# Performance work log

Hardware: AMD Instinct MI355X
Metric: run time of the kernel (lower is better)

Reference implementation:

```python
import jax, jax.numpy as jnp
import numpy as np

H = 256   # hidden_dim
S = 16    # d_state
B = 2
N = 8192
LN_EPS = 1e-5


def setup_inputs() -> dict:
    key = jax.random.key(0)
    ks = jax.random.split(key, 12)
    std = 1.0 / np.sqrt(H)
    inp = {
        'x': jax.random.normal(ks[0], (B, N, H), dtype=jnp.float32),
        'in_w': jax.random.normal(ks[1], (2 * H, H), dtype=jnp.float32) * std,
        'in_b': jax.random.normal(ks[2], (2 * H,), dtype=jnp.float32) * std,
        'xp_w': jax.random.normal(ks[3], (2 * S + 1, H), dtype=jnp.float32) * std,
        'xp_b': jax.random.normal(ks[4], (2 * S + 1,), dtype=jnp.float32) * std,
        'dt_w': jax.random.normal(ks[5], (H, 1), dtype=jnp.float32),
        'dt_b': jax.random.normal(ks[6], (H,), dtype=jnp.float32),
        'A_log': jnp.log(jnp.broadcast_to(jnp.arange(1, S + 1, dtype=jnp.float32), (H, S))),
        'D': jnp.ones((H,), dtype=jnp.float32),
        'out_w': jax.random.normal(ks[7], (H, H), dtype=jnp.float32) * std,
        'out_b': jax.random.normal(ks[8], (H,), dtype=jnp.float32) * std,
        'ln_g': jnp.ones((H,), dtype=jnp.float32),
        'ln_b': jnp.zeros((H,), dtype=jnp.float32),
    }
    return inp


def reference(x, in_w, in_b, xp_w, xp_b, dt_w, dt_b, A_log, D, out_w, out_b, ln_g, ln_b):
    # x: (B, N, H). Dropout is identity in eval mode.
    residual = x
    xz = jnp.einsum('bnh,kh->bnk', x, in_w) + in_b            # (B,N,2H)
    x_inner, z = xz[..., :H], xz[..., H:]
    x_dbl = jnp.einsum('bnh,kh->bnk', x_inner, xp_w) + xp_b   # (B,N,2S+1)
    dt_raw = x_dbl[..., :1]
    B_raw = x_dbl[..., 1:S + 1]                               # (B,N,S)
    C_raw = x_dbl[..., S + 1:]                                # (B,N,S)
    dt = jax.nn.softplus(dt_raw * dt_w[:, 0] + dt_b)          # (B,N,H)
    # NOTE: the original computes dA = exp(dt * A) but never uses it; A_log
    # does not affect the output, so we skip materializing dA.
    dB = dt[..., None] * B_raw[:, :, None, :]                 # (B,N,H,S)
    h = jnp.cumsum(x_inner[..., None] * dB, axis=1)           # (B,N,H,S)
    y = jnp.einsum('bnhs,bns->bnh', h, C_raw) + D * x_inner   # (B,N,H)
    y = y * jax.nn.silu(z)
    out = jnp.einsum('bnh,kh->bnk', y, out_w) + out_b
    r = out + residual
    mu = jnp.mean(r, axis=-1, keepdims=True)
    var = jnp.mean((r - mu) ** 2, axis=-1, keepdims=True)
    return ln_g * (r - mu) * jax.lax.rsqrt(var + LN_EPS) + ln_b
```

## Files before the change

### kernel.cpp

```cpp
#include <hip/hip_runtime.h>
#include <hip/hip_bf16.h>


#define HD 256
#define SD 16
#define NSEQ 8192
#define NBATCH 2
#define BN (NBATCH * NSEQ)
#define CHUNK 32
#define NCHUNK (NSEQ / CHUNK)
#define NGRP 16
#define GSZ (NCHUNK / NGRP)
#define LN_EPS 1e-5f
#define UST 40
#define PST 257

#define NIW (2 * HD * HD)
#define NXP (48 * HD)
#define NOW (HD * HD)

typedef __hip_bfloat16 bf16;
typedef __attribute__((ext_vector_type(8))) short bf16x8;
typedef __attribute__((ext_vector_type(4))) short short4v;
typedef __attribute__((ext_vector_type(4))) float f32x4;
typedef __attribute__((ext_vector_type(4))) unsigned int uint4v;
typedef __attribute__((ext_vector_type(2))) unsigned int uint2v;

__device__ __forceinline__ float b2f(bf16 v) { return __bfloat162float(v); }
__device__ __forceinline__ short f2bs(float f) {
  union { bf16 b; short s; } u;
  u.b = __float2bfloat16(f);
  return u.s;
}
__device__ __forceinline__ unsigned int pack2(float a, float b) {
  return (unsigned int)(unsigned short)f2bs(a) |
         ((unsigned int)(unsigned short)f2bs(b) << 16);
}
__device__ __forceinline__ bf16x8 cvt_frag(const float* p) {
  bf16x8 r;
#pragma unroll
  for (int j = 0; j < 8; ++j) r[j] = f2bs(p[j]);
  return r;
}
__device__ __forceinline__ float softplus_f(float a) {
  return (a > 20.f) ? a : __logf(1.f + __expf(a));
}

__global__ __launch_bounds__(256) void k0_weights(
    const float* __restrict__ in_w, const float* __restrict__ xp_w,
    const float* __restrict__ out_w, bf16* __restrict__ wbin,
    bf16* __restrict__ wbxp, bf16* __restrict__ wbout)
{
  const int base = (blockIdx.x * 256 + threadIdx.x) * 4;
  if (base < NIW) {
    f32x4 v = *(const f32x4*)(in_w + base);
    *(short4v*)((short*)wbin + base) =
        short4v{f2bs(v[0]), f2bs(v[1]), f2bs(v[2]), f2bs(v[3])};
  } else if (base < NIW + NXP) {
    const int off = base - NIW;
    short4v s;
    if (off < 33 * HD) {
      f32x4 v = *(const f32x4*)(xp_w + off);
      s = short4v{f2bs(v[0]), f2bs(v[1]), f2bs(v[2]), f2bs(v[3])};
    } else {
      s = short4v{0, 0, 0, 0};
    }
    *(short4v*)((short*)wbxp + off) = s;
  } else if (base < NIW + NXP + NOW) {
    const int off = base - NIW - NXP;
    f32x4 v = *(const f32x4*)(out_w + off);
    *(short4v*)((short*)wbout + off) =
        short4v{f2bs(v[0]), f2bs(v[1]), f2bs(v[2]), f2bs(v[3])};
  }
}

__global__ __launch_bounds__(256) void k1_gemm(
    const float* __restrict__ x, const bf16* __restrict__ wbin,
    const float* __restrict__ in_b, bf16* __restrict__ xib,
    bf16* __restrict__ zb)
{
  __shared__ __align__(16) char smem[128 * 264 * 2];
  bf16* At = (bf16*)smem;
  float* Ct = (float*)smem;

  const int tid = threadIdx.x;
  const int rt = blockIdx.x & 127, ct = blockIdx.x >> 7;
  const int R0 = rt * 128, C0 = ct * 128;
  const int wave = tid >> 6, lane = tid & 63, q = lane >> 4, l16 = lane & 15;

#pragma unroll
  for (int it = 0; it < 16; ++it) {
    const int f = tid + it * 256;
    const int row = f >> 5, g = f & 31;
    bf16x8 v = cvt_frag(x + (size_t)(R0 + row) * HD + g * 8);
    *(bf16x8*)(At + row * 264 + g * 8) = v;
  }
  __syncthreads();

  const int rowHalf = (wave & 1) * 64;
  const int colHalf = (wave >> 1) * 64;
  f32x4 acc[4][4] = {};
  const bf16* bp = wbin + (size_t)(C0 + colHalf + l16) * HD + q * 8;
#pragma unroll
  for (int k = 0; k < HD; k += 32) {
    bf16x8 a[4], b[4];
#pragma unroll
    for (int i = 0; i < 4; ++i)
      a[i] = *(const bf16x8*)(At + (rowHalf + i * 16 + l16) * 264 + k + q * 8);
#pragma unroll
    for (int j = 0; j < 4; ++j)
      b[j] = *(const bf16x8*)(bp + (size_t)j * 16 * HD + k);
#pragma unroll
    for (int i = 0; i < 4; ++i)
#pragma unroll
      for (int j = 0; j < 4; ++j)
        acc[i][j] = __builtin_amdgcn_mfma_f32_16x16x32_bf16(a[i], b[j], acc[i][j], 0, 0, 0);
  }
  __syncthreads();

#pragma unroll
  for (int j = 0; j < 4; ++j) {
    const int col = colHalf + j * 16 + l16;
    const float bias = in_b[C0 + col];
#pragma unroll
    for (int i = 0; i < 4; ++i)
#pragma unroll
      for (int r = 0; r < 4; ++r)
        Ct[(rowHalf + i * 16 + q * 4 + r) * 132 + col] = acc[i][j][r] + bias;
  }
  __syncthreads();

  bf16* dst = (C0 < HD) ? xib : zb;
  const int Cd = (C0 < HD) ? C0 : (C0 - HD);
#pragma unroll
  for (int it = 0; it < 8; ++it) {
    const int f = tid + it * 256;
    const int row = f >> 4, g = f & 15;
    bf16x8 v = cvt_frag(Ct + row * 132 + g * 8);
    *(bf16x8*)(dst + (size_t)(R0 + row) * HD + Cd + g * 8) = v;
  }
}

__global__ __launch_bounds__(256) void kS_xp_sum(
    const bf16* __restrict__ xib, const bf16* __restrict__ wbxp,
    const float* __restrict__ xp_b, const float* __restrict__ dt_w,
    const float* __restrict__ dt_b, float* __restrict__ dbc,
    float* __restrict__ Mc)
{
  __shared__ __align__(16) bf16 xt[32 * 264];
  __shared__ __align__(16) bf16 wp[48 * 264];
  __shared__ __align__(16) float sdbc[32][33];
  __shared__ __align__(16) bf16 sBt[16 * UST];
  __shared__ __align__(16) bf16 Ut[256 * UST];
  const int tid = threadIdx.x;
  const int wave = tid >> 6, lane = tid & 63, q = lane >> 4, l16 = lane & 15;
  const int cix = blockIdx.x;
  const int R0 = cix * CHUNK;

#pragma unroll
  for (int it = 0; it < 4; ++it) {
    const int f = tid + it * 256, row = f >> 5, g = f & 31;
    *(bf16x8*)(xt + row * 264 + g * 8) =
        *(const bf16x8*)(xib + (size_t)(R0 + row) * HD + g * 8);
  }
#pragma unroll
  for (int it = 0; it < 6; ++it) {
    const int f = tid + it * 256, row = f >> 5, g = f & 31;
    *(bf16x8*)(wp + row * 264 + g * 8) =
        *(const bf16x8*)(wbxp + (size_t)row * HD + g * 8);
  }
  __syncthreads();

  if (wave < 2) {
    f32x4 pacc[3] = {};
#pragma unroll
    for (int k = 0; k < HD; k += 32) {
      bf16x8 af = *(const bf16x8*)(xt + (wave * 16 + l16) * 264 + k + q * 8);
#pragma unroll
      for (int t = 0; t < 3; ++t) {
        bf16x8 bfr = *(const bf16x8*)(wp + (t * 16 + l16) * 264 + k + q * 8);
        pacc[t] = __builtin_amdgcn_mfma_f32_16x16x32_bf16(af, bfr, pacc[t], 0, 0, 0);
      }
    }
#pragma unroll
    for (int t = 0; t < 3; ++t) {
      const int col = t * 16 + l16;
      if (col < 33) {
        const float bias = xp_b[col];
#pragma unroll
        for (int r = 0; r < 4; ++r) {
          const int row = wave * 16 + q * 4 + r;
          const float v = pacc[t][r] + bias;
          sdbc[row][col] = v;
          if (col >= 1 && col < 17)
            *((short*)sBt + (col - 1) * UST + row) = f2bs(v);
        }
      }
    }
  }
  __syncthreads();

  {
    const float* sflat = &sdbc[0][0];
    for (int idx = tid; idx < CHUNK * 33; idx += 256)
      dbc[(size_t)R0 * 33 + idx] = sflat[idx];
  }
  {
    const int h = tid;
    const float dtw = dt_w[h], dtb = dt_b[h];
    unsigned int up[16];
#pragma unroll
    for (int n2 = 0; n2 < 16; ++n2) {
      const int n = 2 * n2;
      const float xv0 = b2f(xt[n * 264 + h]);
      const float xv1 = b2f(xt[(n + 1) * 264 + h]);
      const float u0 = xv0 * softplus_f(sdbc[n][0] * dtw + dtb);
      const float u1 = xv1 * softplus_f(sdbc[n + 1][0] * dtw + dtb);
      up[n2] = pack2(u0, u1);
    }
    uint4v* dst = (uint4v*)(Ut + h * UST);
#pragma unroll
    for (int j = 0; j < 4; ++j)
      dst[j] = uint4v{up[4 * j], up[4 * j + 1], up[4 * j + 2], up[4 * j + 3]};
  }
  __syncthreads();

  {
    bf16x8 af = *(const bf16x8*)(sBt + l16 * UST + q * 8);
    f32x4 macc[4] = {};
#pragma unroll
    for (int c4 = 0; c4 < 4; ++c4) {
      const int ct = wave * 4 + c4;
      bf16x8 bu = *(const bf16x8*)(Ut + (ct * 16 + l16) * UST + q * 8);
      macc[c4] = __builtin_amdgcn_mfma_f32_16x16x32_bf16(af, bu, macc[c4], 0, 0, 0);
    }
    float* mbase = Mc + (size_t)cix * 4096;
#pragma unroll
    for (int c4 = 0; c4 < 4; ++c4) {
      const int h = (wave * 4 + c4) * 16 + l16;
#pragma unroll
      for (int r = 0; r < 4; ++r)
        mbase[(q * 4 + r) * HD + h] = macc[c4][r];
    }
  }
}

__global__ __launch_bounds__(256) void k4a_prefix_local(
    float* __restrict__ Mc, float* __restrict__ Gs)
{
  const int tid = blockIdx.x * 256 + threadIdx.x;
  const int b = tid >> 16;
  const int g = (tid >> 12) & (NGRP - 1);
  const int hs = tid & 4095;
  float run = 0.f;
#pragma unroll
  for (int i = 0; i < GSZ; ++i) {
    const size_t idx = ((size_t)(b * NCHUNK + g * GSZ + i)) * 4096 + hs;
    const float v = Mc[idx];
    Mc[idx] = run;
    run += v;
  }
  Gs[((size_t)(b * NGRP + g)) * 4096 + hs] = run;
}

__global__ __launch_bounds__(256) void k4b_prefix_groups(float* __restrict__ Gs)
{
  const int tid = blockIdx.x * 256 + threadIdx.x;
  const int b = tid >> 12;
  const int hs = tid & 4095;
  float run = 0.f;
#pragma unroll
  for (int g = 0; g < NGRP; ++g) {
    const size_t idx = ((size_t)(b * NGRP + g)) * 4096 + hs;
    const float v = Gs[idx];
    Gs[idx] = run;
    run += v;
  }
}

__global__ __launch_bounds__(256) void k56_scan_out_ln(
    const bf16* __restrict__ xib, const bf16* __restrict__ zb,
    const float* __restrict__ dbc, const float* __restrict__ dt_w,
    const float* __restrict__ dt_b, const float* __restrict__ Dv,
    const float* __restrict__ Mc, const float* __restrict__ Gs,
    const bf16* __restrict__ wbout, const float* __restrict__ out_b,
    const float* __restrict__ x, const float* __restrict__ ln_g,
    const float* __restrict__ ln_b, float* __restrict__ out)
{
  __shared__ __align__(16) char un[53376];
  bf16* Ut  = (bf16*)un;
  bf16* Hst = (bf16*)(un + 20480);
  bf16* Ctl = (bf16*)(un + 40960);
  bf16* Tt  = (bf16*)(un + 43520);
  bf16* yb  = (bf16*)un;
  float* pt = (float*)(un + 20480);
  __shared__ float sdbc[32][33];

  const int tid = threadIdx.x;
  const int wave = tid >> 6, lane = tid & 63, q = lane >> 4, l16 = lane & 15;
  const int cix = blockIdx.x;
  const int R0 = cix * CHUNK;
  const int b = cix >> 8;
  const int cchunk = cix & 255;

  {
    float* sflat = &sdbc[0][0];
    for (int idx = tid; idx < CHUNK * 33; idx += 256)
      sflat[idx] = dbc[(size_t)R0 * 33 + idx];
  }
  __syncthreads();

  {
    const int n = tid >> 3;
    const int m0 = (tid & 7) * 4;
    float cn[SD];
#pragma unroll
    for (int s = 0; s < SD; ++s) cn[s] = sdbc[n][17 + s];
    short4v tv;
#pragma unroll
    for (int mm = 0; mm < 4; ++mm) {
      const int m = m0 + mm;
      float t = 0.f;
#pragma unroll
      for (int s = 0; s < SD; ++s) t += cn[s] * sdbc[m][1 + s];
      tv[mm] = (m <= n) ? f2bs(t) : (short)0;
    }
    *(short4v*)((short*)Tt + n * 32 + m0) = tv;
  }
  {
    const int n = tid >> 3, k0 = (tid & 7) * 4;
    float v[4];
#pragma unroll
    for (int j = 0; j < 4; ++j) {
      const int k = k0 + j;
      v[j] = (k < SD) ? sdbc[n][17 + k] : 0.f;
    }
    *(uint2v*)((short*)Ctl + n * UST + k0) = uint2v{pack2(v[0], v[1]), pack2(v[2], v[3])};
  }
  {
    const int h = tid;
    const float* mp = Mc + (size_t)cix * 4096 + h;
    const float* gp = Gs + ((size_t)(b * NGRP + cchunk / GSZ)) * 4096 + h;
    unsigned int hp[8];
#pragma unroll
    for (int s2 = 0; s2 < 8; ++s2) {
      const int s = 2 * s2;
      hp[s2] = pack2(mp[s * HD] + gp[s * HD], mp[(s + 1) * HD] + gp[(s + 1) * HD]);
    }
    uint4v* hd = (uint4v*)(Hst + h * UST);
    hd[0] = uint4v{hp[0], hp[1], hp[2], hp[3]};
    hd[1] = uint4v{hp[4], hp[5], hp[6], hp[7]};
    hd[2] = uint4v{0, 0, 0, 0};
    hd[3] = uint4v{0, 0, 0, 0};
  }
  {
    const int h = tid;
    const float dtw = dt_w[h], dtb = dt_b[h];
    unsigned int up[16];
#pragma unroll
    for (int n2 = 0; n2 < 16; ++n2) {
      const int n = 2 * n2;
      const float xv0 = b2f(xib[(size_t)(R0 + n) * HD + h]);
      const float xv1 = b2f(xib[(size_t)(R0 + n + 1) * HD + h]);
      const float u0 = xv0 * softplus_f(sdbc[n][0] * dtw + dtb);
      const float u1 = xv1 * softplus_f(sdbc[n + 1][0] * dtw + dtb);
      up[n2] = pack2(u0, u1);
    }
    uint4v* dst = (uint4v*)(Ut + h * UST);
#pragma unroll
    for (int j = 0; j < 4; ++j)
      dst[j] = uint4v{up[4 * j], up[4 * j + 1], up[4 * j + 2], up[4 * j + 3]};
  }
  __syncthreads();

  f32x4 acc[2][4] = {};
  {
    bf16x8 aT0 = *(const bf16x8*)(Tt + l16 * 32 + q * 8);
    bf16x8 aT1 = *(const bf16x8*)(Tt + (16 + l16) * 32 + q * 8);
    bf16x8 aC0 = *(const bf16x8*)(Ctl + l16 * UST + q * 8);
    bf16x8 aC1 = *(const bf16x8*)(Ctl + (16 + l16) * UST + q * 8);
#pragma unroll
    for (int c4 = 0; c4 < 4; ++c4) {
      const int ct = wave * 4 + c4;
      bf16x8 bu = *(const bf16x8*)(Ut + (ct * 16 + l16) * UST + q * 8);
      bf16x8 bh = *(const bf16x8*)(Hst + (ct * 16 + l16) * UST + q * 8);
      acc[0][c4] = __builtin_amdgcn_mfma_f32_16x16x32_bf16(aT0, bu, acc[0][c4], 0, 0, 0);
      acc[0][c4] = __builtin_amdgcn_mfma_f32_16x16x32_bf16(aC0, bh, acc[0][c4], 0, 0, 0);
      acc[1][c4] = __builtin_amdgcn_mfma_f32_16x16x32_bf16(aT1, bu, acc[1][c4], 0, 0, 0);
      acc[1][c4] = __builtin_amdgcn_mfma_f32_16x16x32_bf16(aC1, bh, acc[1][c4], 0, 0, 0);
    }
  }
  __syncthreads();

  {
#pragma unroll
    for (int c4 = 0; c4 < 4; ++c4) {
      const int h = (wave * 4 + c4) * 16 + l16;
      const float dh = Dv[h];
#pragma unroll
      for (int rt = 0; rt < 2; ++rt)
#pragma unroll
        for (int r = 0; r < 4; ++r) {
          const int n = rt * 16 + q * 4 + r;
          const size_t grow = (size_t)(R0 + n) * HD + h;
          const float xv = b2f(xib[grow]);
          const float zv = b2f(zb[grow]);
          const float yv = acc[rt][c4][r] + dh * xv;
          const float sig = 1.f / (1.f + __expf(-zv));
          ((short*)yb)[n * 264 + h] = f2bs(yv * zv * sig);
        }
    }
  }
  __syncthreads();

  const int cw = wave * 64;
  f32x4 oacc[2][4] = {};
#pragma unroll
  for (int k = 0; k < HD; k += 32) {
    bf16x8 a0 = *(const bf16x8*)(yb + l16 * 264 + k + q * 8);
    bf16x8 a1 = *(const bf16x8*)(yb + (16 + l16) * 264 + k + q * 8);
#pragma unroll
    for (int t = 0; t < 4; ++t) {
      bf16x8 bfr = *(const bf16x8*)(wbout + (size_t)(cw + t * 16 + l16) * HD + k + q * 8);
      oacc[0][t] = __builtin_amdgcn_mfma_f32_16x16x32_bf16(a0, bfr, oacc[0][t], 0, 0, 0);
      oacc[1][t] = __builtin_amdgcn_mfma_f32_16x16x32_bf16(a1, bfr, oacc[1][t], 0, 0, 0);
    }
  }
#pragma unroll
  for (int t = 0; t < 4; ++t) {
    const int col = cw + t * 16 + l16;
    const float bias = out_b[col];
#pragma unroll
    for (int rt = 0; rt < 2; ++rt)
#pragma unroll
      for (int r = 0; r < 4; ++r) {
        const int row = rt * 16 + q * 4 + r;
        pt[row * PST + col] = oacc[rt][t][r] + bias + x[(size_t)(R0 + row) * HD + col];
      }
  }
  __syncthreads();

#pragma unroll
  for (int rr = 0; rr < 8; ++rr) {
    const int row = wave * 8 + rr;
    float p = 0.f;
#pragma unroll
    for (int j = 0; j < 4; ++j) p += pt[row * PST + lane + 64 * j];
#pragma unroll
    for (int off = 32; off > 0; off >>= 1) p += __shfl_xor(p, off);
    const float mu = p * (1.f / 256.f);
    float v2 = 0.f;
#pragma unroll
    for (int j = 0; j < 4; ++j) {
      const float d = pt[row * PST + lane + 64 * j] - mu;
      v2 += d * d;
    }
#pragma unroll
    for (int off = 32; off > 0; off >>= 1) v2 += __shfl_xor(v2, off);
    const float rstd = rsqrtf(v2 * (1.f / 256.f) + LN_EPS);
    const size_t base = (size_t)(R0 + row) * HD;
#pragma unroll
    for (int j = 0; j < 4; ++j) {
      const int cc = lane + 64 * j;
      out[base + cc] = ln_g[cc] * (pt[row * PST + cc] - mu) * rstd + ln_b[cc];
    }
  }
}

extern "C" void kernel_launch(void* const* d_in, const int* in_sizes, int n_in,
                              void* d_out, int out_size, void* d_ws, size_t ws_size,
                              hipStream_t stream)
{
  const float* x     = (const float*)d_in[0];
  const float* in_w  = (const float*)d_in[1];
  const float* in_b  = (const float*)d_in[2];
  const float* xp_w  = (const float*)d_in[3];
  const float* xp_b  = (const float*)d_in[4];
  const float* dt_w  = (const float*)d_in[5];
  const float* dt_b  = (const float*)d_in[6];
  const float* Dv    = (const float*)d_in[8];
  const float* out_w = (const float*)d_in[9];
  const float* out_b = (const float*)d_in[10];
  const float* ln_g  = (const float*)d_in[11];
  const float* ln_b  = (const float*)d_in[12];

  char* ws = (char*)d_ws;
  bf16*  xib   = (bf16*)(ws);
  bf16*  zb    = (bf16*)(ws +  8388608);
  float* dbc   = (float*)(ws + 16777216);
  float* Mc    = (float*)(ws + 18939904);
  float* Gs    = (float*)(ws + 27328512);
  bf16*  wbin  = (bf16*)(ws + 27852800);
  bf16*  wbxp  = (bf16*)(ws + 28114944);
  bf16*  wbout = (bf16*)(ws + 28139520);
  float* out   = (float*)d_out;

  hipLaunchKernelGGL(k0_weights, dim3((NIW + NXP + NOW) / 1024), dim3(256),
                     0, stream, in_w, xp_w, out_w, wbin, wbxp, wbout);
  hipLaunchKernelGGL(k1_gemm, dim3(512), dim3(256), 0, stream,
                     x, wbin, in_b, xib, zb);
  hipLaunchKernelGGL(kS_xp_sum, dim3(BN / CHUNK), dim3(256), 0, stream,
                     xib, wbxp, xp_b, dt_w, dt_b, dbc, Mc);
  hipLaunchKernelGGL(k4a_prefix_local, dim3(NBATCH * NGRP * 4096 / 256),
                     dim3(256), 0, stream, Mc, Gs);
  hipLaunchKernelGGL(k4b_prefix_groups, dim3(NBATCH * 4096 / 256), dim3(256),
                     0, stream, Gs);
  hipLaunchKernelGGL(k56_scan_out_ln, dim3(BN / CHUNK), dim3(256), 0, stream,
                     xib, zb, dbc, dt_w, dt_b, Dv, Mc, Gs,
                     wbout, out_b, x, ln_g, ln_b, out);
}
```

Measured before the change: 142.1 us.

## Double block size to 512 threads in GEMM, chunk-sum and scan-output kernels

Three main kernels move from 256 to 512 threads per block, and the work is repartitioned across eight waves instead of four. In the input GEMM each wave now owns a 32x64 tile, while the scan and output kernels split the state and time dimensions across two thread halves. The goal is more wavefronts per block to hide latency, plus smaller per-thread register tiles. The cost is that each wave gets less MFMA work to amortise its fragment loads, and the larger blocks may limit how many blocks fit on a CU.

```diff
diff --git a/kernel.cpp b/kernel.cpp
--- a/kernel.cpp
+++ b/kernel.cpp
@@ -24,7 +24,6 @@
 typedef __attribute__((ext_vector_type(4))) short short4v;
 typedef __attribute__((ext_vector_type(4))) float f32x4;
 typedef __attribute__((ext_vector_type(4))) unsigned int uint4v;
-typedef __attribute__((ext_vector_type(2))) unsigned int uint2v;
 
 __device__ __forceinline__ float b2f(bf16 v) { return __bfloat162float(v); }
 __device__ __forceinline__ short f2bs(float f) {
@@ -74,7 +73,7 @@
   }
 }
 
-__global__ __launch_bounds__(256) void k1_gemm(
+__global__ __launch_bounds__(512) void k1_gemm(
     const float* __restrict__ x, const bf16* __restrict__ wbin,
     const float* __restrict__ in_b, bf16* __restrict__ xib,
     bf16* __restrict__ zb)
@@ -89,29 +88,29 @@
   const int wave = tid >> 6, lane = tid & 63, q = lane >> 4, l16 = lane & 15;
 
 #pragma unroll
-  for (int it = 0; it < 16; ++it) {
-    const int f = tid + it * 256;
+  for (int it = 0; it < 8; ++it) {
+    const int f = tid + it * 512;
     const int row = f >> 5, g = f & 31;
     bf16x8 v = cvt_frag(x + (size_t)(R0 + row) * HD + g * 8);
     *(bf16x8*)(At + row * 264 + g * 8) = v;
   }
   __syncthreads();
 
-  const int rowHalf = (wave & 1) * 64;
-  const int colHalf = (wave >> 1) * 64;
-  f32x4 acc[4][4] = {};
-  const bf16* bp = wbin + (size_t)(C0 + colHalf + l16) * HD + q * 8;
+  const int rowQ = (wave & 3) * 32;
+  const int colH = (wave >> 2) * 64;
+  f32x4 acc[2][4] = {};
+  const bf16* bp = wbin + (size_t)(C0 + colH + l16) * HD + q * 8;
 #pragma unroll
   for (int k = 0; k < HD; k += 32) {
-    bf16x8 a[4], b[4];
-#pragma unroll
-    for (int i = 0; i < 4; ++i)
-      a[i] = *(const bf16x8*)(At + (rowHalf + i * 16 + l16) * 264 + k + q * 8);
+    bf16x8 a[2], b[4];
+#pragma unroll
+    for (int i = 0; i < 2; ++i)
+      a[i] = *(const bf16x8*)(At + (rowQ + i * 16 + l16) * 264 + k + q * 8);
 #pragma unroll
     for (int j = 0; j < 4; ++j)
       b[j] = *(const bf16x8*)(bp + (size_t)j * 16 * HD + k);
 #pragma unroll
-    for (int i = 0; i < 4; ++i)
+    for (int i = 0; i < 2; ++i)
 #pragma unroll
       for (int j = 0; j < 4; ++j)
         acc[i][j] = __builtin_amdgcn_mfma_f32_16x16x32_bf16(a[i], b[j], acc[i][j], 0, 0, 0);
@@ -120,28 +119,28 @@
 
 #pragma unroll
   for (int j = 0; j < 4; ++j) {
-    const int col = colHalf + j * 16 + l16;
+    const int col = colH + j * 16 + l16;
     const float bias = in_b[C0 + col];
 #pragma unroll
-    for (int i = 0; i < 4; ++i)
+    for (int i = 0; i < 2; ++i)
 #pragma unroll
       for (int r = 0; r < 4; ++r)
-        Ct[(rowHalf + i * 16 + q * 4 + r) * 132 + col] = acc[i][j][r] + bias;
+        Ct[(rowQ + i * 16 + q * 4 + r) * 132 + col] = acc[i][j][r] + bias;
   }
   __syncthreads();
 
   bf16* dst = (C0 < HD) ? xib : zb;
   const int Cd = (C0 < HD) ? C0 : (C0 - HD);
 #pragma unroll
-  for (int it = 0; it < 8; ++it) {
-    const int f = tid + it * 256;
+  for (int it = 0; it < 4; ++it) {
+    const int f = tid + it * 512;
     const int row = f >> 4, g = f & 15;
     bf16x8 v = cvt_frag(Ct + row * 132 + g * 8);
     *(bf16x8*)(dst + (size_t)(R0 + row) * HD + Cd + g * 8) = v;
   }
 }
 
-__global__ __launch_bounds__(256) void kS_xp_sum(
+__global__ __launch_bounds__(512) void kS_xp_sum(
     const bf16* __restrict__ xib, const bf16* __restrict__ wbxp,
     const float* __restrict__ xp_b, const float* __restrict__ dt_w,
     const float* __restrict__ dt_b, float* __restrict__ dbc,
@@ -158,14 +157,14 @@
   const int R0 = cix * CHUNK;
 
 #pragma unroll
-  for (int it = 0; it < 4; ++it) {
-    const int f = tid + it * 256, row = f >> 5, g = f & 31;
+  for (int it = 0; it < 2; ++it) {
+    const int f = tid + it * 512, row = f >> 5, g = f & 31;
     *(bf16x8*)(xt + row * 264 + g * 8) =
         *(const bf16x8*)(xib + (size_t)(R0 + row) * HD + g * 8);
   }
 #pragma unroll
-  for (int it = 0; it < 6; ++it) {
-    const int f = tid + it * 256, row = f >> 5, g = f & 31;
+  for (int it = 0; it < 3; ++it) {
+    const int f = tid + it * 512, row = f >> 5, g = f & 31;
     *(bf16x8*)(wp + row * 264 + g * 8) =
         *(const bf16x8*)(wbxp + (size_t)row * HD + g * 8);
   }
@@ -202,45 +201,45 @@
 
   {
     const float* sflat = &sdbc[0][0];
-    for (int idx = tid; idx < CHUNK * 33; idx += 256)
+    for (int idx = tid; idx < CHUNK * 33; idx += 512)
       dbc[(size_t)R0 * 33 + idx] = sflat[idx];
   }
   {
-    const int h = tid;
+    const int h = tid & 255;
+    const int sh = tid >> 8;
     const float dtw = dt_w[h], dtb = dt_b[h];
-    unsigned int up[16];
-#pragma unroll
-    for (int n2 = 0; n2 < 16; ++n2) {
-      const int n = 2 * n2;
+    unsigned int up[8];
+#pragma unroll
+    for (int n2 = 0; n2 < 8; ++n2) {
+      const int n = sh * 16 + 2 * n2;
       const float xv0 = b2f(xt[n * 264 + h]);
       const float xv1 = b2f(xt[(n + 1) * 264 + h]);
       const float u0 = xv0 * softplus_f(sdbc[n][0] * dtw + dtb);
       const float u1 = xv1 * softplus_f(sdbc[n + 1][0] * dtw + dtb);
       up[n2] = pack2(u0, u1);
     }
-    uint4v* dst = (uint4v*)(Ut + h * UST);
-#pragma unroll
-    for (int j = 0; j < 4; ++j)
-      dst[j] = uint4v{up[4 * j], up[4 * j + 1], up[4 * j + 2], up[4 * j + 3]};
+    uint4v* dst = (uint4v*)(Ut + h * UST + sh * 16);
+    dst[0] = uint4v{up[0], up[1], up[2], up[3]};
+    dst[1] = uint4v{up[4], up[5], up[6], up[7]};
   }
   __syncthreads();
 
   {
     bf16x8 af = *(const bf16x8*)(sBt + l16 * UST + q * 8);
-    f32x4 macc[4] = {};
-#pragma unroll
-    for (int c4 = 0; c4 < 4; ++c4) {
-      const int ct = wave * 4 + c4;
+    f32x4 macc[2] = {};
+#pragma unroll
+    for (int c2 = 0; c2 < 2; ++c2) {
+      const int ct = wave * 2 + c2;
       bf16x8 bu = *(const bf16x8*)(Ut + (ct * 16 + l16) * UST + q * 8);
-      macc[c4] = __builtin_amdgcn_mfma_f32_16x16x32_bf16(af, bu, macc[c4], 0, 0, 0);
+      macc[c2] = __builtin_amdgcn_mfma_f32_16x16x32_bf16(af, bu, macc[c2], 0, 0, 0);
     }
     float* mbase = Mc + (size_t)cix * 4096;
 #pragma unroll
-    for (int c4 = 0; c4 < 4; ++c4) {
-      const int h = (wave * 4 + c4) * 16 + l16;
+    for (int c2 = 0; c2 < 2; ++c2) {
+      const int h = (wave * 2 + c2) * 16 + l16;
 #pragma unroll
       for (int r = 0; r < 4; ++r)
-        mbase[(q * 4 + r) * HD + h] = macc[c4][r];
+        mbase[(q * 4 + r) * HD + h] = macc[c2][r];
     }
   }
 }
@@ -278,7 +277,7 @@
   }
 }
 
-__global__ __launch_bounds__(256) void k56_scan_out_ln(
+__global__ __launch_bounds__(512) void k56_scan_out_ln(
     const bf16* __restrict__ xib, const bf16* __restrict__ zb,
     const float* __restrict__ dbc, const float* __restrict__ dt_w,
     const float* __restrict__ dt_b, const float* __restrict__ Dv,
@@ -304,98 +303,91 @@
   const int cchunk = cix & 255;
 
   {
-    float* sflat = &sdbc[0][0];
-    for (int idx = tid; idx < CHUNK * 33; idx += 256)
-      sflat[idx] = dbc[(size_t)R0 * 33 + idx];
-  }
-  __syncthreads();
-
-  {
-    const int n = tid >> 3;
-    const int m0 = (tid & 7) * 4;
-    float cn[SD];
-#pragma unroll
-    for (int s = 0; s < SD; ++s) cn[s] = sdbc[n][17 + s];
-    short4v tv;
-#pragma unroll
-    for (int mm = 0; mm < 4; ++mm) {
-      const int m = m0 + mm;
-      float t = 0.f;
-#pragma unroll
-      for (int s = 0; s < SD; ++s) t += cn[s] * sdbc[m][1 + s];
-      tv[mm] = (m <= n) ? f2bs(t) : (short)0;
-    }
-    *(short4v*)((short*)Tt + n * 32 + m0) = tv;
-  }
-  {
-    const int n = tid >> 3, k0 = (tid & 7) * 4;
-    float v[4];
-#pragma unroll
-    for (int j = 0; j < 4; ++j) {
-      const int k = k0 + j;
-      v[j] = (k < SD) ? sdbc[n][17 + k] : 0.f;
-    }
-    *(uint2v*)((short*)Ctl + n * UST + k0) = uint2v{pack2(v[0], v[1]), pack2(v[2], v[3])};
-  }
-  {
-    const int h = tid;
-    const float* mp = Mc + (size_t)cix * 4096 + h;
-    const float* gp = Gs + ((size_t)(b * NGRP + cchunk / GSZ)) * 4096 + h;
-    unsigned int hp[8];
-#pragma unroll
-    for (int s2 = 0; s2 < 8; ++s2) {
+    const int h = tid & 255;
+    const int sh = tid >> 8;
+    const float* mp = Mc + (size_t)cix * 4096 + sh * 8 * HD + h;
+    const float* gp = Gs + ((size_t)(b * NGRP + cchunk / GSZ)) * 4096 + sh * 8 * HD + h;
+    unsigned int hp[4];
+#pragma unroll
+    for (int s2 = 0; s2 < 4; ++s2) {
       const int s = 2 * s2;
       hp[s2] = pack2(mp[s * HD] + gp[s * HD], mp[(s + 1) * HD] + gp[(s + 1) * HD]);
     }
     uint4v* hd = (uint4v*)(Hst + h * UST);
-    hd[0] = uint4v{hp[0], hp[1], hp[2], hp[3]};
-    hd[1] = uint4v{hp[4], hp[5], hp[6], hp[7]};
-    hd[2] = uint4v{0, 0, 0, 0};
-    hd[3] = uint4v{0, 0, 0, 0};
-  }
-  {
-    const int h = tid;
+    hd[sh] = uint4v{hp[0], hp[1], hp[2], hp[3]};
+    hd[2 + sh] = uint4v{0, 0, 0, 0};
+  }
+  {
+    float* sflat = &sdbc[0][0];
+    for (int idx = tid; idx < CHUNK * 33; idx += 512)
+      sflat[idx] = dbc[(size_t)R0 * 33 + idx];
+  }
+  __syncthreads();
+
+  {
+    const int n = tid >> 4;
+    const int m0 = (tid & 15) * 2;
+    float cn[SD];
+#pragma unroll
+    for (int s = 0; s < SD; ++s) cn[s] = sdbc[n][17 + s];
+    float t0 = 0.f, t1 = 0.f;
+#pragma unroll
+    for (int s = 0; s < SD; ++s) {
+      t0 += cn[s] * sdbc[m0][1 + s];
+      t1 += cn[s] * sdbc[m0 + 1][1 + s];
+    }
+    *(unsigned int*)((short*)Tt + n * 32 + m0) =
+        pack2((m0 <= n) ? t0 : 0.f, (m0 + 1 <= n) ? t1 : 0.f);
+  }
+  {
+    const int n = tid >> 4, k0 = (tid & 15) * 2;
+    const float v0 = (k0 < SD) ? sdbc[n][17 + k0] : 0.f;
+    const float v1 = (k0 + 1 < SD) ? sdbc[n][17 + k0 + 1] : 0.f;
+    *(unsigned int*)((short*)Ctl + n * UST + k0) = pack2(v0, v1);
+  }
+  {
+    const int h = tid & 255;
+    const int sh = tid >> 8;
     const float dtw = dt_w[h], dtb = dt_b[h];
-    unsigned int up[16];
-#pragma unroll
-    for (int n2 = 0; n2 < 16; ++n2) {
-      const int n = 2 * n2;
+    unsigned int up[8];
+#pragma unroll
+    for (int n2 = 0; n2 < 8; ++n2) {
+      const int n = sh * 16 + 2 * n2;
       const float xv0 = b2f(xib[(size_t)(R0 + n) * HD + h]);
       const float xv1 = b2f(xib[(size_t)(R0 + n + 1) * HD + h]);
       const float u0 = xv0 * softplus_f(sdbc[n][0] * dtw + dtb);
       const float u1 = xv1 * softplus_f(sdbc[n + 1][0] * dtw + dtb);
       up[n2] = pack2(u0, u1);
     }
-    uint4v* dst = (uint4v*)(Ut + h * UST);
-#pragma unroll
-    for (int j = 0; j < 4; ++j)
-      dst[j] = uint4v{up[4 * j], up[4 * j + 1], up[4 * j + 2], up[4 * j + 3]};
-  }
-  __syncthreads();
-
-  f32x4 acc[2][4] = {};
+    uint4v* dst = (uint4v*)(Ut + h * UST + sh * 16);
+    dst[0] = uint4v{up[0], up[1], up[2], up[3]};
+    dst[1] = uint4v{up[4], up[5], up[6], up[7]};
+  }
+  __syncthreads();
+
+  f32x4 acc[2][2] = {};
   {
     bf16x8 aT0 = *(const bf16x8*)(Tt + l16 * 32 + q * 8);
     bf16x8 aT1 = *(const bf16x8*)(Tt + (16 + l16) * 32 + q * 8);
     bf16x8 aC0 = *(const bf16x8*)(Ctl + l16 * UST + q * 8);
     bf16x8 aC1 = *(const bf16x8*)(Ctl + (16 + l16) * UST + q * 8);
 #pragma unroll
-    for (int c4 = 0; c4 < 4; ++c4) {
-      const int ct = wave * 4 + c4;
+    for (int c2 = 0; c2 < 2; ++c2) {
+      const int ct = wave * 2 + c2;
       bf16x8 bu = *(const bf16x8*)(Ut + (ct * 16 + l16) * UST + q * 8);
       bf16x8 bh = *(const bf16x8*)(Hst + (ct * 16 + l16) * UST + q * 8);
-      acc[0][c4] = __builtin_amdgcn_mfma_f32_16x16x32_bf16(aT0, bu, acc[0][c4], 0, 0, 0);
-      acc[0][c4] = __builtin_amdgcn_mfma_f32_16x16x32_bf16(aC0, bh, acc[0][c4], 0, 0, 0);
-      acc[1][c4] = __builtin_amdgcn_mfma_f32_16x16x32_bf16(aT1, bu, acc[1][c4], 0, 0, 0);
-      acc[1][c4] = __builtin_amdgcn_mfma_f32_16x16x32_bf16(aC1, bh, acc[1][c4], 0, 0, 0);
-    }
-  }
-  __syncthreads();
-
-  {
-#pragma unroll
-    for (int c4 = 0; c4 < 4; ++c4) {
-      const int h = (wave * 4 + c4) * 16 + l16;
+      acc[0][c2] = __builtin_amdgcn_mfma_f32_16x16x32_bf16(aT0, bu, acc[0][c2], 0, 0, 0);
+      acc[0][c2] = __builtin_amdgcn_mfma_f32_16x16x32_bf16(aC0, bh, acc[0][c2], 0, 0, 0);
+      acc[1][c2] = __builtin_amdgcn_mfma_f32_16x16x32_bf16(aT1, bu, acc[1][c2], 0, 0, 0);
+      acc[1][c2] = __builtin_amdgcn_mfma_f32_16x16x32_bf16(aC1, bh, acc[1][c2], 0, 0, 0);
+    }
+  }
+  __syncthreads();
+
+  {
+#pragma unroll
+    for (int c2 = 0; c2 < 2; ++c2) {
+      const int h = (wave * 2 + c2) * 16 + l16;
       const float dh = Dv[h];
 #pragma unroll
       for (int rt = 0; rt < 2; ++rt)
@@ -405,7 +397,7 @@
           const size_t grow = (size_t)(R0 + n) * HD + h;
           const float xv = b2f(xib[grow]);
           const float zv = b2f(zb[grow]);
-          const float yv = acc[rt][c4][r] + dh * xv;
+          const float yv = acc[rt][c2][r] + dh * xv;
           const float sig = 1.f / (1.f + __expf(-zv));
           ((short*)yb)[n * 264 + h] = f2bs(yv * zv * sig);
         }
@@ -413,21 +405,21 @@
   }
   __syncthreads();
 
-  const int cw = wave * 64;
-  f32x4 oacc[2][4] = {};
+  const int cw = wave * 32;
+  f32x4 oacc[2][2] = {};
 #pragma unroll
   for (int k = 0; k < HD; k += 32) {
     bf16x8 a0 = *(const bf16x8*)(yb + l16 * 264 + k + q * 8);
     bf16x8 a1 = *(const bf16x8*)(yb + (16 + l16) * 264 + k + q * 8);
 #pragma unroll
-    for (int t = 0; t < 4; ++t) {
+    for (int t = 0; t < 2; ++t) {
       bf16x8 bfr = *(const bf16x8*)(wbout + (size_t)(cw + t * 16 + l16) * HD + k + q * 8);
       oacc[0][t] = __builtin_amdgcn_mfma_f32_16x16x32_bf16(a0, bfr, oacc[0][t], 0, 0, 0);
       oacc[1][t] = __builtin_amdgcn_mfma_f32_16x16x32_bf16(a1, bfr, oacc[1][t], 0, 0, 0);
     }
   }
 #pragma unroll
-  for (int t = 0; t < 4; ++t) {
+  for (int t = 0; t < 2; ++t) {
     const int col = cw + t * 16 + l16;
     const float bias = out_b[col];
 #pragma unroll
@@ -441,8 +433,8 @@
   __syncthreads();
 
 #pragma unroll
-  for (int rr = 0; rr < 8; ++rr) {
-    const int row = wave * 8 + rr;
+  for (int rr = 0; rr < 4; ++rr) {
+    const int row = wave * 4 + rr;
     float p = 0.f;
 #pragma unroll
     for (int j = 0; j < 4; ++j) p += pt[row * PST + lane + 64 * j];
@@ -497,15 +489,15 @@
 
   hipLaunchKernelGGL(k0_weights, dim3((NIW + NXP + NOW) / 1024), dim3(256),
                      0, stream, in_w, xp_w, out_w, wbin, wbxp, wbout);
-  hipLaunchKernelGGL(k1_gemm, dim3(512), dim3(256), 0, stream,
+  hipLaunchKernelGGL(k1_gemm, dim3(512), dim3(512), 0, stream,
                      x, wbin, in_b, xib, zb);
-  hipLaunchKernelGGL(kS_xp_sum, dim3(BN / CHUNK), dim3(256), 0, stream,
+  hipLaunchKernelGGL(kS_xp_sum, dim3(BN / CHUNK), dim3(512), 0, stream,
                      xib, wbxp, xp_b, dt_w, dt_b, dbc, Mc);
   hipLaunchKernelGGL(k4a_prefix_local, dim3(NBATCH * NGRP * 4096 / 256),
                      dim3(256), 0, stream, Mc, Gs);
   hipLaunchKernelGGL(k4b_prefix_groups, dim3(NBATCH * 4096 / 256), dim3(256),
                      0, stream, Gs);
-  hipLaunchKernelGGL(k56_scan_out_ln, dim3(BN / CHUNK), dim3(256), 0, stream,
+  hipLaunchKernelGGL(k56_scan_out_ln, dim3(BN / CHUNK), dim3(512), 0, stream,
                      xib, zb, dbc, dt_w, dt_b, Dv, Mc, Gs,
                      wbout, out_b, x, ln_g, ln_b, out);
 }
```

New measurement: 145.5 us. 1.02x slower.
